# Kernel tuning notes

Hardware: AMD Instinct MI355X
Metric: run time of the kernel (lower is better)

## Reference

```python
import jax, jax.numpy as jnp
import numpy as np

N = 8192        # number of nodes (adjacency is N x N)
F_IN = 256      # in_features
F_OUT = 256     # out_features


def setup_inputs() -> dict:
    key = jax.random.key(0)
    k_x, k_adj, k_kernel, k_bias, k_beta = jax.random.split(key, 5)
    x = jax.random.normal(k_x, (N, F_IN), dtype=jnp.float32)
    adj = jax.random.uniform(k_adj, (N, N), dtype=jnp.float32)  # dense non-negative adjacency buffer
    # xavier-uniform-like scale for the kernel
    limit = float(np.sqrt(6.0 / (F_IN + F_OUT)))
    kernel = jax.random.uniform(k_kernel, (F_IN, F_OUT), dtype=jnp.float32, minval=-limit, maxval=limit)
    bias = 0.01 * jax.random.normal(k_bias, (F_OUT,), dtype=jnp.float32)
    beta = 0.01 * jax.random.normal(k_beta, (N,), dtype=jnp.float32)
    return {"x": x, "adj": adj, "kernel": kernel, "bias": bias, "beta": beta}


def reference(x, adj, kernel, bias, beta):
    # Original: diag(1/(rowsum(adj)+beta)) @ (adj + diag(beta)) @ x @ kernel + bias
    # Fused form: row-scale and diagonal-add applied without materializing NxN diag matrices.
    scale = jnp.reciprocal(jnp.sum(adj, axis=1) + beta)          # [N]
    agg = adj @ x + beta[:, None] * x                             # (adj + diag(beta)) @ x  -> [N, F_IN]
    return (scale[:, None] * agg) @ kernel + bias                 # [N, F_OUT]
```

## Files before the change

kernel.cpp:

```cpp
#include <hip/hip_runtime.h>
#include <hip/hip_bf16.h>


typedef __attribute__((ext_vector_type(8))) short  short8;
typedef __attribute__((ext_vector_type(4))) float  floatx4;

#define N_NODES 8192
#define F_DIM   256
#define BK      64
#define NSTEPS  (N_NODES / BK)

#define ASYNC16(g, l)                                                          \
  __builtin_amdgcn_global_load_lds(                                           \
      (const __attribute__((address_space(1))) void*)(g),                     \
      (__attribute__((address_space(3))) void*)(l), 16, 0, 0)

__device__ __forceinline__ unsigned short f2bf(float f) {
  unsigned u = __float_as_uint(f);
  return (unsigned short)((u + 0x7FFFu + ((u >> 16) & 1u)) >> 16);
}

__device__ __forceinline__ short8 pack_bf16x8(floatx4 a, floatx4 b) {
  short8 r;
  r[0] = (short)f2bf(a.x);
  r[1] = (short)f2bf(a.y);
  r[2] = (short)f2bf(a.z);
  r[3] = (short)f2bf(a.w);
  r[4] = (short)f2bf(b.x);
  r[5] = (short)f2bf(b.y);
  r[6] = (short)f2bf(b.z);
  r[7] = (short)f2bf(b.w);
  return r;
}

__global__ __launch_bounds__(256) void tile_bf16_kernel(
    const float* __restrict__ src, unsigned short* __restrict__ dst, int K) {
  const int Nn = F_DIM;
  int cid = blockIdx.x * 256 + threadIdx.x;
  int per_kblk = Nn * 4;
  int kblk = cid / per_kblk;
  int rem  = cid - kblk * per_kblk;
  int n16 = rem >> 6;
  int kg  = (rem >> 4) & 3;
  int nl  = rem & 15;
  int n = n16 * 16 + nl;
  int k = kblk * 32 + kg * 8;
  const float* s = src + (size_t)k * Nn + n;
  floatx4 v0, v1;
  v0.x = s[0];
  v0.y = s[(size_t)Nn];
  v0.z = s[(size_t)2 * Nn];
  v0.w = s[(size_t)3 * Nn];
  v1.x = s[(size_t)4 * Nn];
  v1.y = s[(size_t)5 * Nn];
  v1.z = s[(size_t)6 * Nn];
  v1.w = s[(size_t)7 * Nn];
  *(short8*)(dst + (size_t)cid * 8) = pack_bf16x8(v0, v1);
}

__global__ __launch_bounds__(512, 2) void fused_kernel(
    const float* __restrict__ adj, const unsigned short* __restrict__ xbt,
    const float* __restrict__ x, const float* __restrict__ beta,
    const float* __restrict__ bias, const unsigned short* __restrict__ wbt,
    float* __restrict__ out) {
  __shared__ __attribute__((aligned(16))) char smem[123136];
  float* sscale = (float*)(smem + 122880);
  float* sbeta  = (float*)(smem + 123008);

  const int tid = threadIdx.x;
  const int w   = tid >> 6;
  const int l   = tid & 63;
  const int kq  = l >> 4;
  const int ml  = l & 15;
  const int wm  = w >> 2;
  const int wn  = w & 3;
  const int m0  = blockIdx.x * 32;

  const int arow = tid >> 4;
  const int agrp = tid & 15;
  const float* asrc_base =
      adj + (size_t)(m0 + arow) * N_NODES + ((agrp ^ (arow & 7)) << 2);
  const unsigned short* bsrc_base = xbt + (size_t)tid * 8;

  const int frow = wm * 16 + ml;
  int aoff[2][2];
#pragma unroll
  for (int kb = 0; kb < 2; ++kb) {
    int g0 = kb * 8 + kq * 2;
    aoff[kb][0] = frow * 64 + (((g0)     ^ (frow & 7)) << 2);
    aoff[kb][1] = frow * 64 + (((g0 + 1) ^ (frow & 7)) << 2);
  }
  const int boffbase = wn * 2048 + kq * 128 + ml * 8;

  floatx4 acc[4];
  const floatx4 zf4 = {0.f, 0.f, 0.f, 0.f};
#pragma unroll
  for (int nf = 0; nf < 4; ++nf) acc[nf] = zf4;
  float rsum = 0.f;

#pragma unroll
  for (int s = 0; s < 2; ++s) {
    ASYNC16(asrc_base + s * BK, smem + s * 8192 + (w << 10));
    const unsigned short* bs = bsrc_base + (size_t)s * 16384;
    char* bd = smem + 24576 + s * 32768 + (w << 10);
#pragma unroll
    for (int q = 0; q < 4; ++q) ASYNC16(bs + q * 4096, bd + q * 8192);
  }

  auto compute = [&](int cur) {
    const float* Af = (const float*)(smem + cur * 8192);
    const unsigned short* Bf = (const unsigned short*)(smem + 24576 + cur * 32768);
    short8 af[2];
#pragma unroll
    for (int kb = 0; kb < 2; ++kb) {
      floatx4 a0 = *(const floatx4*)(Af + aoff[kb][0]);
      floatx4 a1 = *(const floatx4*)(Af + aoff[kb][1]);
      if (wn == 0)
        rsum += (a0.x + a0.y + a0.z + a0.w) + (a1.x + a1.y + a1.z + a1.w);
      af[kb] = pack_bf16x8(a0, a1);
    }
#pragma unroll
    for (int nf = 0; nf < 4; ++nf) {
      short8 b0 = *(const short8*)(Bf + boffbase + nf * 512);
      short8 b1 = *(const short8*)(Bf + 8192 + boffbase + nf * 512);
      acc[nf] = __builtin_amdgcn_mfma_f32_16x16x32_bf16(af[0], b0, acc[nf], 0, 0, 0);
      acc[nf] = __builtin_amdgcn_mfma_f32_16x16x32_bf16(af[1], b1, acc[nf], 0, 0, 0);
    }
  };

  int cur = 0, stg = 2;
  for (int s = 0; s < NSTEPS - 2; ++s) {
    asm volatile("s_waitcnt vmcnt(5)\n\ts_barrier" ::: "memory");
    ASYNC16(asrc_base + (s + 2) * BK, smem + stg * 8192 + (w << 10));
    {
      const unsigned short* bs = bsrc_base + (size_t)(s + 2) * 16384;
      char* bd = smem + 24576 + stg * 32768 + (w << 10);
#pragma unroll
      for (int q = 0; q < 4; ++q) ASYNC16(bs + q * 4096, bd + q * 8192);
    }
    compute(cur);
    cur = cur + 1; if (cur == 3) cur = 0;
    stg = stg + 1; if (stg == 3) stg = 0;
  }
  for (int s = NSTEPS - 2; s < NSTEPS; ++s) {
    asm volatile("s_waitcnt vmcnt(0)\n\ts_barrier" ::: "memory");
    compute(cur);
    cur = cur + 1; if (cur == 3) cur = 0;
  }

  __syncthreads();

  {
    const float* xs = x + (size_t)m0 * F_DIM + tid * 4;
    char* xd = smem + 24576 + (w << 10);
#pragma unroll
    for (int q = 0; q < 4; ++q) ASYNC16(xs + q * 2048, xd + q * 8192);
  }
  if (wn == 0) {
    float rs = rsum;
    rs += __shfl_xor(rs, 16);
    rs += __shfl_xor(rs, 32);
    if (l < 16) {
      float b = beta[m0 + wm * 16 + l];
      sbeta[wm * 16 + l]  = b;
      sscale[wm * 16 + l] = 1.0f / (rs + b);
    }
  }
  __syncthreads();

  const float* xl = (const float*)(smem + 24576);
  unsigned short* G = (unsigned short*)smem;
#pragma unroll
  for (int nf = 0; nf < 4; ++nf) {
    int col = wn * 64 + nf * 16 + ml;
    int chunk = col >> 3;
#pragma unroll
    for (int r = 0; r < 4; ++r) {
      int row = wm * 16 + kq * 4 + r;
      float g = sscale[row] * (acc[nf][r] + sbeta[row] * xl[row * F_DIM + col]);
      G[row * 256 + (((chunk ^ (row & 7)) << 3) | (col & 7))] = f2bf(g);
    }
  }
  __syncthreads();

  floatx4 acc2[4];
#pragma unroll
  for (int nf = 0; nf < 4; ++nf) acc2[nf] = zf4;
  const int grow = wm * 16 + ml;
#pragma unroll
  for (int s2 = 0; s2 < 8; ++s2) {
    short8 ag = *(const short8*)(G + grow * 256 +
                                 (((s2 * 4 + kq) ^ (grow & 7)) << 3));
    const unsigned short* wb = wbt + s2 * 8192 + boffbase;
#pragma unroll
    for (int nf = 0; nf < 4; ++nf) {
      short8 bv = *(const short8*)(wb + nf * 512);
      acc2[nf] = __builtin_amdgcn_mfma_f32_16x16x32_bf16(ag, bv, acc2[nf], 0, 0, 0);
    }
  }
#pragma unroll
  for (int nf = 0; nf < 4; ++nf) {
    int col = wn * 64 + nf * 16 + ml;
    float bv = bias[col];
#pragma unroll
    for (int r = 0; r < 4; ++r) {
      int row = m0 + wm * 16 + kq * 4 + r;
      out[(size_t)row * F_DIM + col] = acc2[nf][r] + bv;
    }
  }
}

extern "C" void kernel_launch(void* const* d_in, const int* in_sizes, int n_in,
                              void* d_out, int out_size, void* d_ws, size_t ws_size,
                              hipStream_t stream) {
  const float* x    = (const float*)d_in[0];
  const float* adj  = (const float*)d_in[1];
  const float* kern = (const float*)d_in[2];
  const float* bias = (const float*)d_in[3];
  const float* beta = (const float*)d_in[4];
  float* out = (float*)d_out;

  char* ws = (char*)d_ws;
  unsigned short* xbt = (unsigned short*)ws;
  unsigned short* wbt = xbt + (size_t)N_NODES * F_DIM;

  tile_bf16_kernel<<<(N_NODES * F_DIM / 8) / 256, 256, 0, stream>>>(x, xbt, N_NODES);
  tile_bf16_kernel<<<(F_DIM * F_DIM / 8) / 256, 256, 0, stream>>>(kern, wbt, F_DIM);
  fused_kernel<<<256, 512, 0, stream>>>(adj, xbt, x, beta, bias, wbt, out);
}
```

Baseline: 416.9 us.

## Convert adj to bf16 once per tile in registers and retile warps 2x2

Each thread now loads its adj fragment into registers, accumulates the row sum and writes a bf16-packed copy to shared memory, so the fp32-to-bf16 conversion and the row-sum happen once per element. Before, four warps converted the same A fragment redundantly. Each warp now owns a 32x32 output tile (two M fragments by two N fragments) instead of 16x64, so A fragments are reused across N and B reads are smaller. The A shared buffer halves in size, and the pipeline is unrolled by three with explicit waitcnt and barrier placement. The cost is extra register pressure from holding the prefetched A register, plus more complex manual synchronization.

```diff
diff --git a/kernel.cpp b/kernel.cpp
--- a/kernel.cpp
+++ b/kernel.cpp
@@ -3,6 +3,7 @@
 
 
 typedef __attribute__((ext_vector_type(8))) short  short8;
+typedef __attribute__((ext_vector_type(4))) short  bf16x4;
 typedef __attribute__((ext_vector_type(4))) float  floatx4;
 
 #define N_NODES 8192
@@ -58,155 +59,200 @@
   *(short8*)(dst + (size_t)cid * 8) = pack_bf16x8(v0, v1);
 }
 
+#define AB(i) (smem + (i) * 4096)
+#define BB(i) (smem + 12288 + (i) * 32768)
+
+#define STAGE_B(sidx, c)                                                       \
+  {                                                                            \
+    const unsigned short* bs_ = bsrc + (size_t)(sidx) * 16384;                 \
+    char* bd_ = BB(c) + (w << 10);                                             \
+    ASYNC16(bs_,          bd_);                                                \
+    ASYNC16(bs_ +  4096,  bd_ +  8192);                                        \
+    ASYNC16(bs_ +  8192,  bd_ + 16384);                                        \
+    ASYNC16(bs_ + 12288,  bd_ + 24576);                                        \
+  }
+
+#define WRITE_A(c)                                                             \
+  {                                                                            \
+    rsum += (areg.x + areg.y) + (areg.z + areg.w);                             \
+    bf16x4 pk_;                                                                \
+    pk_[0] = (short)f2bf(areg.x);                                              \
+    pk_[1] = (short)f2bf(areg.y);                                              \
+    pk_[2] = (short)f2bf(areg.z);                                              \
+    pk_[3] = (short)f2bf(areg.w);                                              \
+    *(bf16x4*)(AB(c) + awoff) = pk_;                                           \
+  }
+
+#define MFMA16(a, b, c) __builtin_amdgcn_mfma_f32_16x16x32_bf16(a, b, c, 0, 0, 0)
+
+#define COMPUTE(c)                                                             \
+  {                                                                            \
+    const char* Ab_ = AB(c);                                                   \
+    const char* Bb_ = BB(c);                                                   \
+    short8 a00 = *(const short8*)(Ab_ + aoff00);                               \
+    short8 a01 = *(const short8*)(Ab_ + aoff01);                               \
+    short8 a10 = *(const short8*)(Ab_ + aoff10);                               \
+    short8 a11 = *(const short8*)(Ab_ + aoff11);                               \
+    short8 b00 = *(const short8*)(Bb_ + boff00);                               \
+    short8 b01 = *(const short8*)(Bb_ + boff01);                               \
+    short8 b10 = *(const short8*)(Bb_ + boff10);                               \
+    short8 b11 = *(const short8*)(Bb_ + boff11);                               \
+    acc[0][0] = MFMA16(a00, b00, acc[0][0]);                                   \
+    acc[1][0] = MFMA16(a01, b00, acc[1][0]);                                   \
+    acc[0][1] = MFMA16(a00, b01, acc[0][1]);                                   \
+    acc[1][1] = MFMA16(a01, b01, acc[1][1]);                                   \
+    acc[0][0] = MFMA16(a10, b10, acc[0][0]);                                   \
+    acc[1][0] = MFMA16(a11, b10, acc[1][0]);                                   \
+    acc[0][1] = MFMA16(a10, b11, acc[0][1]);                                   \
+    acc[1][1] = MFMA16(a11, b11, acc[1][1]);                                   \
+  }
+
+#define FULL_ITER(sidx, c)                                                     \
+  asm volatile("s_waitcnt vmcnt(4)" ::: "memory");                             \
+  WRITE_A((c + 1) % 3);                                                        \
+  areg = *(const floatx4*)(asrc + (size_t)((sidx) + 2) * BK);                  \
+  asm volatile("s_waitcnt lgkmcnt(0)" ::: "memory");                           \
+  asm volatile("s_barrier" ::: "memory");                                      \
+  STAGE_B((sidx) + 2, (c + 2) % 3);                                           \
+  COMPUTE(c);
+
 __global__ __launch_bounds__(512, 2) void fused_kernel(
     const float* __restrict__ adj, const unsigned short* __restrict__ xbt,
     const float* __restrict__ x, const float* __restrict__ beta,
     const float* __restrict__ bias, const unsigned short* __restrict__ wbt,
     float* __restrict__ out) {
-  __shared__ __attribute__((aligned(16))) char smem[123136];
-  float* sscale = (float*)(smem + 122880);
-  float* sbeta  = (float*)(smem + 123008);
+  __shared__ __attribute__((aligned(16))) char smem[110592];
+  float* sscale = (float*)(smem + 49152);
+  float* sbeta  = (float*)(smem + 49280);
 
   const int tid = threadIdx.x;
   const int w   = tid >> 6;
   const int l   = tid & 63;
   const int kq  = l >> 4;
   const int ml  = l & 15;
-  const int wm  = w >> 2;
-  const int wn  = w & 3;
+  const int r7  = ml & 7;
   const int m0  = blockIdx.x * 32;
 
   const int arow = tid >> 4;
-  const int agrp = tid & 15;
-  const float* asrc_base =
-      adj + (size_t)(m0 + arow) * N_NODES + ((agrp ^ (arow & 7)) << 2);
-  const unsigned short* bsrc_base = xbt + (size_t)tid * 8;
-
-  const int frow = wm * 16 + ml;
-  int aoff[2][2];
-#pragma unroll
-  for (int kb = 0; kb < 2; ++kb) {
-    int g0 = kb * 8 + kq * 2;
-    aoff[kb][0] = frow * 64 + (((g0)     ^ (frow & 7)) << 2);
-    aoff[kb][1] = frow * 64 + (((g0 + 1) ^ (frow & 7)) << 2);
-  }
-  const int boffbase = wn * 2048 + kq * 128 + ml * 8;
-
-  floatx4 acc[4];
+  const int akc  = tid & 15;
+  const float* asrc = adj + (size_t)(m0 + arow) * N_NODES + akc * 4;
+  const int awoff = arow * 128 + ((((akc >> 1) ^ (arow & 7))) << 4) + (akc & 1) * 8;
+  const unsigned short* bsrc = xbt + (size_t)tid * 8;
+
+  const int aoff00 = (0 * 16 + ml) * 128 + (((0 * 4 + kq) ^ r7) << 4);
+  const int aoff01 = (1 * 16 + ml) * 128 + (((0 * 4 + kq) ^ r7) << 4);
+  const int aoff10 = (0 * 16 + ml) * 128 + (((1 * 4 + kq) ^ r7) << 4);
+  const int aoff11 = (1 * 16 + ml) * 128 + (((1 * 4 + kq) ^ r7) << 4);
+  const int boff00 = 0 * 16384 + (w * 2 + 0) * 1024 + kq * 256 + ml * 16;
+  const int boff01 = 0 * 16384 + (w * 2 + 1) * 1024 + kq * 256 + ml * 16;
+  const int boff10 = 1 * 16384 + (w * 2 + 0) * 1024 + kq * 256 + ml * 16;
+  const int boff11 = 1 * 16384 + (w * 2 + 1) * 1024 + kq * 256 + ml * 16;
+
+  floatx4 acc[2][2];
   const floatx4 zf4 = {0.f, 0.f, 0.f, 0.f};
-#pragma unroll
-  for (int nf = 0; nf < 4; ++nf) acc[nf] = zf4;
+  acc[0][0] = zf4; acc[0][1] = zf4; acc[1][0] = zf4; acc[1][1] = zf4;
   float rsum = 0.f;
-
-#pragma unroll
-  for (int s = 0; s < 2; ++s) {
-    ASYNC16(asrc_base + s * BK, smem + s * 8192 + (w << 10));
-    const unsigned short* bs = bsrc_base + (size_t)s * 16384;
-    char* bd = smem + 24576 + s * 32768 + (w << 10);
-#pragma unroll
-    for (int q = 0; q < 4; ++q) ASYNC16(bs + q * 4096, bd + q * 8192);
-  }
-
-  auto compute = [&](int cur) {
-    const float* Af = (const float*)(smem + cur * 8192);
-    const unsigned short* Bf = (const unsigned short*)(smem + 24576 + cur * 32768);
-    short8 af[2];
-#pragma unroll
-    for (int kb = 0; kb < 2; ++kb) {
-      floatx4 a0 = *(const floatx4*)(Af + aoff[kb][0]);
-      floatx4 a1 = *(const floatx4*)(Af + aoff[kb][1]);
-      if (wn == 0)
-        rsum += (a0.x + a0.y + a0.z + a0.w) + (a1.x + a1.y + a1.z + a1.w);
-      af[kb] = pack_bf16x8(a0, a1);
-    }
-#pragma unroll
-    for (int nf = 0; nf < 4; ++nf) {
-      short8 b0 = *(const short8*)(Bf + boffbase + nf * 512);
-      short8 b1 = *(const short8*)(Bf + 8192 + boffbase + nf * 512);
-      acc[nf] = __builtin_amdgcn_mfma_f32_16x16x32_bf16(af[0], b0, acc[nf], 0, 0, 0);
-      acc[nf] = __builtin_amdgcn_mfma_f32_16x16x32_bf16(af[1], b1, acc[nf], 0, 0, 0);
-    }
-  };
-
-  int cur = 0, stg = 2;
-  for (int s = 0; s < NSTEPS - 2; ++s) {
-    asm volatile("s_waitcnt vmcnt(5)\n\ts_barrier" ::: "memory");
-    ASYNC16(asrc_base + (s + 2) * BK, smem + stg * 8192 + (w << 10));
-    {
-      const unsigned short* bs = bsrc_base + (size_t)(s + 2) * 16384;
-      char* bd = smem + 24576 + stg * 32768 + (w << 10);
-#pragma unroll
-      for (int q = 0; q < 4; ++q) ASYNC16(bs + q * 4096, bd + q * 8192);
-    }
-    compute(cur);
-    cur = cur + 1; if (cur == 3) cur = 0;
-    stg = stg + 1; if (stg == 3) stg = 0;
-  }
-  for (int s = NSTEPS - 2; s < NSTEPS; ++s) {
-    asm volatile("s_waitcnt vmcnt(0)\n\ts_barrier" ::: "memory");
-    compute(cur);
-    cur = cur + 1; if (cur == 3) cur = 0;
-  }
+  floatx4 areg;
+
+  areg = *(const floatx4*)(asrc);
+  STAGE_B(0, 0);
+  asm volatile("s_waitcnt vmcnt(4)" ::: "memory");
+  WRITE_A(0);
+  areg = *(const floatx4*)(asrc + BK);
+  STAGE_B(1, 1);
+  asm volatile("s_waitcnt vmcnt(4)" ::: "memory");
+  WRITE_A(1);
+  areg = *(const floatx4*)(asrc + 2 * BK);
+  asm volatile("s_waitcnt lgkmcnt(0)" ::: "memory");
+  asm volatile("s_barrier" ::: "memory");
+  STAGE_B(2, 2);
+  COMPUTE(0);
+
+  for (int t = 0; t < 41; ++t) {
+    const int s0 = 3 * t + 1;
+    FULL_ITER(s0,     1);
+    FULL_ITER(s0 + 1, 2);
+    FULL_ITER(s0 + 2, 0);
+  }
+  FULL_ITER(124, 1);
+  FULL_ITER(125, 2);
+  asm volatile("s_waitcnt vmcnt(4)" ::: "memory");
+  WRITE_A(1);
+  asm volatile("s_waitcnt lgkmcnt(0)" ::: "memory");
+  asm volatile("s_barrier" ::: "memory");
+  COMPUTE(0);
+  asm volatile("s_waitcnt vmcnt(0)" ::: "memory");
+  asm volatile("s_barrier" ::: "memory");
+  COMPUTE(1);
 
   __syncthreads();
 
   {
     const float* xs = x + (size_t)m0 * F_DIM + tid * 4;
-    char* xd = smem + 24576 + (w << 10);
+    char* xd = smem + 16384 + (w << 10);
 #pragma unroll
     for (int q = 0; q < 4; ++q) ASYNC16(xs + q * 2048, xd + q * 8192);
   }
-  if (wn == 0) {
+  {
     float rs = rsum;
-    rs += __shfl_xor(rs, 16);
-    rs += __shfl_xor(rs, 32);
-    if (l < 16) {
-      float b = beta[m0 + wm * 16 + l];
-      sbeta[wm * 16 + l]  = b;
-      sscale[wm * 16 + l] = 1.0f / (rs + b);
+    rs += __shfl_xor(rs, 1);
+    rs += __shfl_xor(rs, 2);
+    rs += __shfl_xor(rs, 4);
+    rs += __shfl_xor(rs, 8);
+    if ((l & 15) == 0) {
+      int row = w * 4 + (l >> 4);
+      float b = beta[m0 + row];
+      sbeta[row]  = b;
+      sscale[row] = 1.0f / (rs + b);
     }
   }
   __syncthreads();
 
-  const float* xl = (const float*)(smem + 24576);
+  const float* xl = (const float*)(smem + 16384);
   unsigned short* G = (unsigned short*)smem;
 #pragma unroll
-  for (int nf = 0; nf < 4; ++nf) {
-    int col = wn * 64 + nf * 16 + ml;
+  for (int nf = 0; nf < 2; ++nf) {
+    int col = w * 32 + nf * 16 + ml;
     int chunk = col >> 3;
 #pragma unroll
-    for (int r = 0; r < 4; ++r) {
-      int row = wm * 16 + kq * 4 + r;
-      float g = sscale[row] * (acc[nf][r] + sbeta[row] * xl[row * F_DIM + col]);
-      G[row * 256 + (((chunk ^ (row & 7)) << 3) | (col & 7))] = f2bf(g);
-    }
+    for (int mf = 0; mf < 2; ++mf)
+#pragma unroll
+      for (int r = 0; r < 4; ++r) {
+        int row = mf * 16 + kq * 4 + r;
+        float g = sscale[row] * (acc[mf][nf][r] + sbeta[row] * xl[row * F_DIM + col]);
+        int slot = (chunk & 24) | ((chunk ^ row) & 7);
+        G[row * 256 + slot * 8 + (col & 7)] = f2bf(g);
+      }
   }
   __syncthreads();
 
-  floatx4 acc2[4];
-#pragma unroll
-  for (int nf = 0; nf < 4; ++nf) acc2[nf] = zf4;
-  const int grow = wm * 16 + ml;
+  floatx4 acc2[2][2];
+  acc2[0][0] = zf4; acc2[0][1] = zf4; acc2[1][0] = zf4; acc2[1][1] = zf4;
 #pragma unroll
   for (int s2 = 0; s2 < 8; ++s2) {
-    short8 ag = *(const short8*)(G + grow * 256 +
-                                 (((s2 * 4 + kq) ^ (grow & 7)) << 3));
-    const unsigned short* wb = wbt + s2 * 8192 + boffbase;
-#pragma unroll
-    for (int nf = 0; nf < 4; ++nf) {
-      short8 bv = *(const short8*)(wb + nf * 512);
-      acc2[nf] = __builtin_amdgcn_mfma_f32_16x16x32_bf16(ag, bv, acc2[nf], 0, 0, 0);
-    }
-  }
-#pragma unroll
-  for (int nf = 0; nf < 4; ++nf) {
-    int col = wn * 64 + nf * 16 + ml;
+    int c = s2 * 4 + kq;
+    int sl = (c & 24) | ((c ^ ml) & 7);
+    short8 ag0 = *(const short8*)(G + (ml)      * 256 + sl * 8);
+    short8 ag1 = *(const short8*)(G + (16 + ml) * 256 + sl * 8);
+    const unsigned short* wb = wbt + s2 * 8192 + (w * 2) * 512 + kq * 128 + ml * 8;
+    short8 wv0 = *(const short8*)(wb);
+    short8 wv1 = *(const short8*)(wb + 512);
+    acc2[0][0] = MFMA16(ag0, wv0, acc2[0][0]);
+    acc2[1][0] = MFMA16(ag1, wv0, acc2[1][0]);
+    acc2[0][1] = MFMA16(ag0, wv1, acc2[0][1]);
+    acc2[1][1] = MFMA16(ag1, wv1, acc2[1][1]);
+  }
+#pragma unroll
+  for (int nf = 0; nf < 2; ++nf) {
+    int col = w * 32 + nf * 16 + ml;
     float bv = bias[col];
 #pragma unroll
-    for (int r = 0; r < 4; ++r) {
-      int row = m0 + wm * 16 + kq * 4 + r;
-      out[(size_t)row * F_DIM + col] = acc2[nf][r] + bv;
-    }
+    for (int mf = 0; mf < 2; ++mf)
+#pragma unroll
+      for (int r = 0; r < 4; ++r) {
+        int row = m0 + mf * 16 + kq * 4 + r;
+        out[(size_t)row * F_DIM + col] = acc2[mf][nf][r] + bv;
+      }
   }
 }
 
```

New measurement: 440.2 us. 5.6% more time.
